# Optimization experiments

Measured on AMD Instinct MI355X. Metric: run time of the kernel, lower is better.

The kernel has to match this reference:

```python
import jax, jax.numpy as jnp
import numpy as np
import math

IN_C, OUT_C = 64, 128
OUT_C1 = int((OUT_C - IN_C) * 0.3 + IN_C)  # 83
OUT_C2 = int((OUT_C - IN_C) * 0.6 + IN_C)  # 102
OUT_C3 = OUT_C                              # 128
RESIDUE_RATIO = 0.5
R_RES = math.sqrt(RESIDUE_RATIO)
R_SC = math.sqrt(1.0 - RESIDUE_RATIO)
PRELU_INIT = 0.25
POST_MEAN = (1.0 - PRELU_INIT) / math.sqrt(2.0 * math.pi)
_POST_EX2 = (1.0 + PRELU_INIT ** 2) / 2.0
POST_STDV = math.sqrt(_POST_EX2 - POST_MEAN ** 2)


def _conv1x1_weight(key, out_c, in_c):
    # torch Conv1d custom init: normal_, then divide by per-out-channel L2 norm
    w = jax.random.normal(key, (out_c, in_c), dtype=jnp.float32)
    norm = jnp.sqrt(jnp.sum(w ** 2, axis=1, keepdims=True) + 1e-8)
    return w / norm


def cprelu(x, w):
    # x: [B, C, N], w: [C]
    y = jnp.where(x >= 0, x, x * w[None, :, None])
    return (y - POST_MEAN) / POST_STDV


def setup_inputs() -> dict:
    key = jax.random.key(0)
    ks = jax.random.split(key, 8)
    x = jax.random.normal(ks[0], (16, IN_C, 8192), dtype=jnp.float32)
    conn = jax.random.uniform(ks[1], (4096, 8192), dtype=jnp.float32)
    return {
        "x": x,
        "conn": conn,
        "w1": _conv1x1_weight(ks[2], OUT_C1, IN_C),
        "b1": jnp.zeros((OUT_C1,), jnp.float32),
        "p1": jnp.full((OUT_C1,), PRELU_INIT, jnp.float32),
        "w2": _conv1x1_weight(ks[3], OUT_C2, OUT_C1),
        "b2": jnp.zeros((OUT_C2,), jnp.float32),
        "p2": jnp.full((OUT_C2,), PRELU_INIT, jnp.float32),
        "wm": _conv1x1_weight(ks[4], OUT_C3, OUT_C2),
        "bm": jnp.zeros((OUT_C3,), jnp.float32),
        "p3": jnp.full((OUT_C3,), PRELU_INIT, jnp.float32),
        "ws": _conv1x1_weight(ks[5], OUT_C, IN_C),
        "bs": jnp.zeros((OUT_C,), jnp.float32),
    }


def _forward(x, conn, w1, b1, p1, w2, b2, p2, wm, bm, p3, ws, bs):
    # self-connection matrix: binary mask of per-row argmax entries (ties kept)
    sc = (conn - jnp.max(conn, axis=1, keepdims=True) >= 0).astype(jnp.float32)

    # residue branch: 1x1 conv -> CPReLU -> 1x1 conv -> CPReLU -> Meshconv -> CPReLU
    h = cprelu(jnp.einsum('bcn,oc->bon', x, w1) + b1[None, :, None], p1)
    h = cprelu(jnp.einsum('bcn,oc->bon', h, w2) + b2[None, :, None], p2)
    h = jnp.einsum('bcn,oc->bon', h, wm) + bm[None, :, None]      # [B, C3, Nin]
    h = jnp.einsum('oi,bci->bco', conn, h)                         # mesh pooling -> [B, C3, Nout]
    res = cprelu(h, p3)

    # shortcut branch: Meshconv with self_connection_matrix (1x1 conv + pooled gather)
    s = jnp.einsum('bcn,oc->bon', x, ws) + bs[None, :, None]       # [B, OUT_C, Nin]
    s = jnp.einsum('oi,bci->bco', sc, s)                           # [B, OUT_C, Nout]

    return s * R_SC + res * R_RES


def reference(x, conn, w1, b1, p1, w2, b2, p2, wm, bm, p3, ws, bs):
    return _forward(x, conn, w1, b1, p1, w2, b2, p2, wm, bm, p3, ws, bs)
```

## Files before the change

### kernel.cpp

```cpp
#include <hip/hip_runtime.h>
#include <hip/hip_bf16.h>
#include <stdint.h>

using bf16x8 = __attribute__((ext_vector_type(8))) __bf16;
using bf16x4 = __attribute__((ext_vector_type(4))) __bf16;
using f32x4  = __attribute__((ext_vector_type(4))) float;

typedef const uint32_t __attribute__((address_space(1)))* gas_ptr;
typedef uint32_t __attribute__((address_space(3)))* las_ptr;

__device__ __forceinline__ void load_lds16(const void* g, void* l) {
    __builtin_amdgcn_global_load_lds((gas_ptr)g, (las_ptr)l, 16, 0, 0);
}

#define PM  0.29920671030107454f
#define PIS 1.5046096f
#define RHALF 0.70710678118654752f

__global__ __launch_bounds__(256) void k_prep(const float* __restrict__ w1,
                                              const float* __restrict__ w2,
                                              const float* __restrict__ wm,
                                              const float* __restrict__ wsw,
                                              __bf16* __restrict__ W1p,
                                              __bf16* __restrict__ W2p,
                                              __bf16* __restrict__ WMp,
                                              __bf16* __restrict__ WSp)
{
    const int id = blockIdx.x * 256 + threadIdx.x;
    const int stride = gridDim.x * 256;
    for (int i = id; i < 96 * 64; i += stride) {
        int oc = i >> 6, ic = i & 63;
        W1p[i] = (__bf16)((oc < 83) ? w1[oc * 64 + ic] : 0.f);
    }
    for (int i = id; i < 112 * 96; i += stride) {
        int oc = i / 96, ic = i % 96;
        W2p[i] = (__bf16)((oc < 102 && ic < 83) ? w2[oc * 83 + ic] : 0.f);
    }
    for (int i = id; i < 128 * 128; i += stride) {
        int oc = i >> 7, ic = i & 127;
        WMp[i] = (__bf16)((ic < 102) ? wm[oc * 102 + ic] : 0.f);
    }
    for (int i = id; i < 128 * 64; i += stride) {
        WSp[i] = (__bf16)wsw[i];
    }
}

__global__ __launch_bounds__(256) void k_conv(const float* __restrict__ conn,
                                              __bf16* __restrict__ cb,
                                              size_t rowstride,
                                              int* __restrict__ cnt,
                                              int* __restrict__ idx)
{
    const int o = blockIdx.x;
    const int t = threadIdx.x;
    const float* row = conn + (size_t)o * 8192;
    float4 v[8];
    float m = -1e30f;
#pragma unroll
    for (int q = 0; q < 8; q++) {
        v[q] = *(const float4*)(row + (size_t)(q * 256 + t) * 4);
        m = fmaxf(m, fmaxf(fmaxf(v[q].x, v[q].y), fmaxf(v[q].z, v[q].w)));
    }
    __syncthreads();
    __bf16* drow = cb + (size_t)o * rowstride;
#pragma unroll
    for (int q = 0; q < 8; q++) {
        bf16x4 w;
        w[0] = (__bf16)v[q].x; w[1] = (__bf16)v[q].y;
        w[2] = (__bf16)v[q].z; w[3] = (__bf16)v[q].w;
        *(bf16x4*)(drow + (size_t)(q * 256 + t) * 4) = w;
    }
#pragma unroll
    for (int off = 32; off > 0; off >>= 1) m = fmaxf(m, __shfl_down(m, off, 64));
    __shared__ float wmax[4];
    __shared__ int scnt;
    if ((t & 63) == 0) wmax[t >> 6] = m;
    if (t == 0) scnt = 0;
    __syncthreads();
    const float rmax = fmaxf(fmaxf(wmax[0], wmax[1]), fmaxf(wmax[2], wmax[3]));
#pragma unroll
    for (int q = 0; q < 8; q++) {
        float vv[4] = {v[q].x, v[q].y, v[q].z, v[q].w};
#pragma unroll
        for (int e = 0; e < 4; e++) {
            if (vv[e] >= rmax) {
                int p = atomicAdd(&scnt, 1);
                if (p < 16) idx[o * 16 + p] = (q * 256 + t) * 4 + e;
            }
        }
    }
    __syncthreads();
    if (t == 0) cnt[o] = scnt < 16 ? scnt : 16;
}

template<int KS>
__device__ __forceinline__ f32x4 mfma_tile(const __bf16* __restrict__ W, int wstride, int mt,
                                           const __bf16* B, int bstride, int nt, int lane)
{
    f32x4 acc = {0.f, 0.f, 0.f, 0.f};
    const int l15 = lane & 15;
    const int kg  = (lane >> 4) << 3;
    const __bf16* wp = W + (mt * 16 + l15) * wstride + kg;
    const __bf16* bp = B + (nt * 16 + l15) * bstride + kg;
#pragma unroll
    for (int ks = 0; ks < KS; ks++) {
        bf16x8 av = *(const bf16x8*)(wp + ks * 32);
        bf16x8 bv = *(const bf16x8*)(bp + ks * 32);
        acc = __builtin_amdgcn_mfma_f32_16x16x32_bf16(av, bv, acc, 0, 0, 0);
    }
    return acc;
}

__global__ __launch_bounds__(256) void k_chain(
    const float* __restrict__ x,
    const float* __restrict__ b1, const float* __restrict__ p1,
    const float* __restrict__ b2, const float* __restrict__ p2,
    const float* __restrict__ bm, const float* __restrict__ bs,
    const __bf16* __restrict__ W1p, const __bf16* __restrict__ W2p,
    const __bf16* __restrict__ WMp, const __bf16* __restrict__ WSp,
    __bf16* __restrict__ h3, __bf16* __restrict__ s_t)
{
    __shared__ __bf16 buf0[64 * 136];
    __shared__ __bf16 un[128 * 72];
    __shared__ float  bl[672];
    __bf16* H1t  = un;
    __bf16* OutT = un;
    float* b1l = bl;       float* p1l = bl + 96;
    float* b2l = bl + 192; float* p2l = bl + 304;
    float* bml = bl + 416; float* bsl = bl + 544;

    const int t = threadIdx.x, lane = t & 63, wid = t >> 6;
    const int b = blockIdx.y;
    const int p0 = blockIdx.x * 64;

    for (int i = t; i < 96; i += 256)  { b1l[i] = (i < 83)  ? b1[i] : 0.f; p1l[i] = (i < 83)  ? p1[i] : 0.f; }
    for (int i = t; i < 112; i += 256) { b2l[i] = (i < 102) ? b2[i] : 0.f; p2l[i] = (i < 102) ? p2[i] : 0.f; }
    for (int i = t; i < 128; i += 256) { bml[i] = bm[i]; bsl[i] = bs[i]; }

    {
        const int p = t & 63;
        const int cg = t >> 6;
#pragma unroll 4
        for (int it = 0; it < 16; it++) {
            int c = it * 4 + cg;
            buf0[p * 72 + c] = (__bf16)x[((size_t)b * 64 + c) * 8192 + p0 + p];
        }
    }
    __syncthreads();

    const int quad4 = (lane >> 4) << 2;
    const int l15 = lane & 15;

    for (int tt = wid; tt < 32; tt += 4) {
        int mt = tt >> 2, nt = tt & 3;
        f32x4 a = mfma_tile<2>(WSp, 64, mt, buf0, 72, nt, lane);
        int ocb = mt * 16 + quad4;
        int pos = nt * 16 + l15;
        bf16x4 ov;
#pragma unroll
        for (int r = 0; r < 4; r++) ov[r] = (__bf16)(a[r] + bsl[ocb + r]);
        *(bf16x4*)(s_t + ((size_t)b * 8192 + p0 + pos) * 128 + ocb) = ov;
    }
    for (int tt = wid; tt < 24; tt += 4) {
        int mt = tt >> 2, nt = tt & 3;
        f32x4 a = mfma_tile<2>(W1p, 64, mt, buf0, 72, nt, lane);
        int ocb = mt * 16 + quad4;
        int pos = nt * 16 + l15;
        bf16x4 ov;
#pragma unroll
        for (int r = 0; r < 4; r++) {
            float v = a[r] + b1l[ocb + r];
            v = (v >= 0.f) ? v : v * p1l[ocb + r];
            ov[r] = (__bf16)((v - PM) * PIS);
        }
        *(bf16x4*)(&H1t[pos * 104 + ocb]) = ov;
    }
    __syncthreads();

    for (int tt = wid; tt < 28; tt += 4) {
        int mt = tt >> 2, nt = tt & 3;
        f32x4 a = mfma_tile<3>(W2p, 96, mt, H1t, 104, nt, lane);
        int ocb = mt * 16 + quad4;
        int pos = nt * 16 + l15;
        bf16x4 ov;
#pragma unroll
        for (int r = 0; r < 4; r++) {
            float v = a[r] + b2l[ocb + r];
            v = (v >= 0.f) ? v : v * p2l[ocb + r];
            ov[r] = (__bf16)((v - PM) * PIS);
        }
        *(bf16x4*)(&buf0[pos * 136 + ocb]) = ov;
    }
    for (int i = t; i < 64 * 16; i += 256) {
        int pos = i >> 4, c = 112 + (i & 15);
        buf0[pos * 136 + c] = (__bf16)0.f;
    }
    __syncthreads();

    for (int tt = wid; tt < 32; tt += 4) {
        int mt = tt >> 2, nt = tt & 3;
        f32x4 a = mfma_tile<4>(WMp, 128, mt, buf0, 136, nt, lane);
        int ocb = mt * 16 + quad4;
        int pos = nt * 16 + l15;
#pragma unroll
        for (int r = 0; r < 4; r++)
            OutT[(ocb + r) * 72 + pos] = (__bf16)(a[r] + bml[ocb + r]);
    }
    __syncthreads();

#pragma unroll
    for (int it = 0; it < 4; it++) {
        int lin = it * 256 + t;
        int ch = lin >> 3, pc = lin & 7;
        bf16x8 v = *(const bf16x8*)(OutT + ch * 72 + pc * 8);
        *(bf16x8*)(h3 + ((size_t)b * 128 + ch) * 8192 + p0 + pc * 8) = v;
    }
}

__global__ __launch_bounds__(256, 4) void k_gemm(const __bf16* __restrict__ A,
                                                 const __bf16* __restrict__ B,
                                                 size_t bstride,
                                                 float* __restrict__ C0,
                                                 float* __restrict__ C1,
                                                 int KH)
{
    __shared__ __bf16 la[128 * 64];
    __shared__ __bf16 lb[128 * 64];
    const int t = threadIdx.x;
    const int lane = t & 63;
    const int wid = t >> 6;
    const int tM = blockIdx.y * 128;
    const int tN = blockIdx.x * 128;
    const int kz = blockIdx.z;
    const int k0 = kz * KH;
    float* __restrict__ C = kz ? C1 : C0;
    const int wm2 = (wid & 1) * 64;
    const int wn2 = (wid >> 1) * 64;

    f32x4 acc[4][4];
    const f32x4 zero = {0.f, 0.f, 0.f, 0.f};
#pragma unroll
    for (int i = 0; i < 4; i++)
#pragma unroll
        for (int j = 0; j < 4; j++) acc[i][j] = zero;

    const int tr = t >> 3;
    const int sc = (t & 7) ^ (tr & 7);
    const __bf16* pA[4];
    const __bf16* pB[4];
#pragma unroll
    for (int i = 0; i < 4; i++) {
        pA[i] = A + (size_t)(tM + i * 32 + tr) * 8192 + k0 + sc * 8;
        pB[i] = B + (size_t)(tN + i * 32 + tr) * bstride + k0 + sc * 8;
    }

    const int l15 = lane & 15;
    const int q = lane >> 4;
    int aoff[4], boff[4];
#pragma unroll
    for (int i = 0; i < 4; i++) {
        int row = wm2 + i * 16 + l15;
        aoff[i] = row * 64 + ((q ^ (row & 7)) * 8);
    }
#pragma unroll
    for (int j = 0; j < 4; j++) {
        int row = wn2 + j * 16 + l15;
        boff[j] = row * 64 + ((q ^ (row & 7)) * 8);
    }

    const int iters = KH >> 6;
    for (int it = 0; it < iters; it++) {
#pragma unroll
        for (int i = 0; i < 4; i++) load_lds16(pA[i], la + (i * 256 + t) * 8);
#pragma unroll
        for (int i = 0; i < 4; i++) load_lds16(pB[i], lb + (i * 256 + t) * 8);
#pragma unroll
        for (int i = 0; i < 4; i++) { pA[i] += 64; pB[i] += 64; }
        __syncthreads();
#pragma unroll
        for (int ks = 0; ks < 2; ks++) {
            bf16x8 af[4], bfr[4];
#pragma unroll
            for (int i = 0; i < 4; i++) af[i]  = *(const bf16x8*)(la + (aoff[i] ^ (ks << 5)));
#pragma unroll
            for (int j = 0; j < 4; j++) bfr[j] = *(const bf16x8*)(lb + (boff[j] ^ (ks << 5)));
#pragma unroll
            for (int i = 0; i < 4; i++)
#pragma unroll
                for (int j = 0; j < 4; j++)
                    acc[i][j] = __builtin_amdgcn_mfma_f32_16x16x32_bf16(af[i], bfr[j], acc[i][j], 0, 0, 0);
        }
        __syncthreads();
    }

    const int quad4 = (lane >> 4) * 4;
#pragma unroll
    for (int i = 0; i < 4; i++) {
        int gm = tM + wm2 + i * 16 + quad4;
#pragma unroll
        for (int j = 0; j < 4; j++) {
            int gn = tN + wn2 + j * 16 + l15;
#pragma unroll
            for (int r = 0; r < 4; r++)
                C[(size_t)(gm + r) * 4096 + gn] = acc[i][j][r];
        }
    }
}

__global__ __launch_bounds__(256) void k_combine(float* __restrict__ out,
                                                 const float* __restrict__ P1,
                                                 int nsplit,
                                                 const __bf16* __restrict__ s_t,
                                                 const int* __restrict__ idx,
                                                 const int* __restrict__ cnt,
                                                 const float* __restrict__ p3)
{
    __shared__ float sp[64][133];
    const int b = blockIdx.y;
    const int o0 = blockIdx.x * 64;
    const int t = threadIdx.x;

    {
        const int ol = t >> 2;
        const int part = t & 3;
        const int o = o0 + ol;
        const int n = cnt[o];
        float acc[32];
#pragma unroll
        for (int j = 0; j < 32; j++) acc[j] = 0.f;
        for (int k = 0; k < n; k++) {
            const int i = idx[o * 16 + k];
            const __bf16* row = s_t + ((size_t)b * 8192 + i) * 128 + part * 32;
#pragma unroll
            for (int j = 0; j < 32; j += 8) {
                bf16x8 v = *(const bf16x8*)(row + j);
#pragma unroll
                for (int u = 0; u < 8; u++) acc[j + u] += (float)v[u];
            }
        }
#pragma unroll
        for (int j = 0; j < 32; j++) sp[ol][part * 32 + j] = acc[j];
    }
    __syncthreads();

    if (nsplit == 2) {
        for (int rr = 0; rr < 32; rr++) {
            const int c = rr * 4 + (t >> 6);
            const int o = t & 63;
            const size_t oi = ((size_t)b * 128 + c) * 4096 + o0 + o;
            float v = out[oi] + P1[oi];
            const float pw = p3[c];
            float y = (v >= 0.f) ? v : v * pw;
            y = (y - PM) * PIS;
            out[oi] = sp[o][c] * RHALF + y * RHALF;
        }
    } else {
        for (int rr = 0; rr < 32; rr++) {
            const int c = rr * 4 + (t >> 6);
            const int o = t & 63;
            const size_t oi = ((size_t)b * 128 + c) * 4096 + o0 + o;
            float v = out[oi];
            const float pw = p3[c];
            float y = (v >= 0.f) ? v : v * pw;
            y = (y - PM) * PIS;
            out[oi] = sp[o][c] * RHALF + y * RHALF;
        }
    }
}

extern "C" void kernel_launch(void* const* d_in, const int* in_sizes, int n_in,
                              void* d_out, int out_size, void* d_ws, size_t ws_size,
                              hipStream_t stream) {
    (void)in_sizes; (void)n_in; (void)out_size;
    const float* x    = (const float*)d_in[0];
    const float* conn = (const float*)d_in[1];
    const float* w1   = (const float*)d_in[2];
    const float* b1   = (const float*)d_in[3];
    const float* p1   = (const float*)d_in[4];
    const float* w2   = (const float*)d_in[5];
    const float* b2   = (const float*)d_in[6];
    const float* p2   = (const float*)d_in[7];
    const float* wm   = (const float*)d_in[8];
    const float* bm   = (const float*)d_in[9];
    const float* p3   = (const float*)d_in[10];
    const float* wsw  = (const float*)d_in[11];
    const float* bs   = (const float*)d_in[12];
    float* out = (float*)d_out;

    char* ws = (char*)d_ws;
    __bf16* h3  = (__bf16*)(ws);
    __bf16* s_t = (__bf16*)(ws + 33554432);
    __bf16* W1p = (__bf16*)(ws + 67108864);
    __bf16* W2p = (__bf16*)(ws + 67108864 + 12288);
    __bf16* WMp = (__bf16*)(ws + 67108864 + 33792);
    __bf16* WSp = (__bf16*)(ws + 67108864 + 66560);
    int* idx = (int*)(ws + 67108864 + 82944);
    int* cnt = (int*)(ws + 67108864 + 82944 + 262144);
    const size_t p1_off    = 67108864 + 82944 + 262144 + 16384;
    float* Pk1 = (float*)(ws + p1_off);
    const size_t connb_off = p1_off + 33554432;

    __bf16* connb;
    size_t  cstride;
    if (ws_size >= connb_off + (size_t)4096 * 8192 * 2) {
        connb = (__bf16*)(ws + connb_off);
        cstride = 8192;
    } else {
        connb = (__bf16*)const_cast<float*>(conn);
        cstride = 16384;
    }
    const int nsplit = (ws_size >= p1_off + 33554432) ? 2 : 1;
    const int KH = 8192 / nsplit;

    k_prep<<<32, 256, 0, stream>>>(w1, w2, wm, wsw, W1p, W2p, WMp, WSp);
    k_conv<<<4096, 256, 0, stream>>>(conn, connb, cstride, cnt, idx);
    k_chain<<<dim3(8192 / 64, 16), 256, 0, stream>>>(x, b1, p1, b2, p2, bm, bs,
                                                     W1p, W2p, WMp, WSp, h3, s_t);
    k_gemm<<<dim3(4096 / 128, 2048 / 128, nsplit), 256, 0, stream>>>(h3, connb, cstride,
                                                                     out, Pk1, KH);
    k_combine<<<dim3(4096 / 64, 16), 256, 0, stream>>>(out, Pk1, nsplit, s_t, idx, cnt, p3);
}
```

Baseline: 485.8 us.

## Split GEMM K four ways, fuse weight prep, stage shortcut stores, vectorize combine

Several changes land together. The weight-prep kernel is folded into the conn conversion kernel, which removes one launch. The shortcut output is staged through LDS so global writes become contiguous 16-byte stores. The main GEMM's K split goes from 2 to 4 when the workspace allows, which adds more blocks but also more partial buffers that must be read back. The combine epilogue is vectorized to float4 and sums up to four partials.

```diff
diff --git a/kernel.cpp b/kernel.cpp
--- a/kernel.cpp
+++ b/kernel.cpp
@@ -17,7 +17,12 @@
 #define PIS 1.5046096f
 #define RHALF 0.70710678118654752f
 
-__global__ __launch_bounds__(256) void k_prep(const float* __restrict__ w1,
+__global__ __launch_bounds__(256) void k_conv(const float* __restrict__ conn,
+                                              __bf16* __restrict__ cb,
+                                              size_t rowstride,
+                                              int* __restrict__ cnt,
+                                              int* __restrict__ idx,
+                                              const float* __restrict__ w1,
                                               const float* __restrict__ w2,
                                               const float* __restrict__ wm,
                                               const float* __restrict__ wsw,
@@ -26,31 +31,6 @@
                                               __bf16* __restrict__ WMp,
                                               __bf16* __restrict__ WSp)
 {
-    const int id = blockIdx.x * 256 + threadIdx.x;
-    const int stride = gridDim.x * 256;
-    for (int i = id; i < 96 * 64; i += stride) {
-        int oc = i >> 6, ic = i & 63;
-        W1p[i] = (__bf16)((oc < 83) ? w1[oc * 64 + ic] : 0.f);
-    }
-    for (int i = id; i < 112 * 96; i += stride) {
-        int oc = i / 96, ic = i % 96;
-        W2p[i] = (__bf16)((oc < 102 && ic < 83) ? w2[oc * 83 + ic] : 0.f);
-    }
-    for (int i = id; i < 128 * 128; i += stride) {
-        int oc = i >> 7, ic = i & 127;
-        WMp[i] = (__bf16)((ic < 102) ? wm[oc * 102 + ic] : 0.f);
-    }
-    for (int i = id; i < 128 * 64; i += stride) {
-        WSp[i] = (__bf16)wsw[i];
-    }
-}
-
-__global__ __launch_bounds__(256) void k_conv(const float* __restrict__ conn,
-                                              __bf16* __restrict__ cb,
-                                              size_t rowstride,
-                                              int* __restrict__ cnt,
-                                              int* __restrict__ idx)
-{
     const int o = blockIdx.x;
     const int t = threadIdx.x;
     const float* row = conn + (size_t)o * 8192;
@@ -91,6 +71,26 @@
     }
     __syncthreads();
     if (t == 0) cnt[o] = scnt < 16 ? scnt : 16;
+
+    if (o < 32) {
+        const int id = o * 256 + t;
+        const int stride = 32 * 256;
+        for (int i = id; i < 96 * 64; i += stride) {
+            int oc = i >> 6, ic = i & 63;
+            W1p[i] = (__bf16)((oc < 83) ? w1[oc * 64 + ic] : 0.f);
+        }
+        for (int i = id; i < 112 * 96; i += stride) {
+            int oc = i / 96, ic = i % 96;
+            W2p[i] = (__bf16)((oc < 102 && ic < 83) ? w2[oc * 83 + ic] : 0.f);
+        }
+        for (int i = id; i < 128 * 128; i += stride) {
+            int oc = i >> 7, ic = i & 127;
+            WMp[i] = (__bf16)((ic < 102) ? wm[oc * 102 + ic] : 0.f);
+        }
+        for (int i = id; i < 128 * 64; i += stride) {
+            WSp[i] = (__bf16)wsw[i];
+        }
+    }
 }
 
 template<int KS>
@@ -123,6 +123,7 @@
     __shared__ __bf16 buf0[64 * 136];
     __shared__ __bf16 un[128 * 72];
     __shared__ float  bl[672];
+    __bf16* OutS = un;
     __bf16* H1t  = un;
     __bf16* OutT = un;
     float* b1l = bl;       float* p1l = bl + 96;
@@ -159,8 +160,21 @@
         bf16x4 ov;
 #pragma unroll
         for (int r = 0; r < 4; r++) ov[r] = (__bf16)(a[r] + bsl[ocb + r]);
-        *(bf16x4*)(s_t + ((size_t)b * 8192 + p0 + pos) * 128 + ocb) = ov;
-    }
+        *(bf16x4*)(&OutS[pos * 132 + ocb]) = ov;
+    }
+    __syncthreads();
+    {
+        __bf16* dst = s_t + ((size_t)b * 8192 + p0) * 128;
+#pragma unroll
+        for (int it = 0; it < 4; it++) {
+            int lin = it * 256 + t;
+            int pos = lin >> 4, c8 = (lin & 15) * 8;
+            bf16x8 v = *(const bf16x8*)(OutS + pos * 132 + c8);
+            *(bf16x8*)(dst + lin * 8) = v;
+        }
+    }
+    __syncthreads();
+
     for (int tt = wid; tt < 24; tt += 4) {
         int mt = tt >> 2, nt = tt & 3;
         f32x4 a = mfma_tile<2>(W1p, 64, mt, buf0, 72, nt, lane);
@@ -221,7 +235,9 @@
                                                  const __bf16* __restrict__ B,
                                                  size_t bstride,
                                                  float* __restrict__ C0,
-                                                 float* __restrict__ C1,
+                                                 float* __restrict__ P1,
+                                                 float* __restrict__ P2,
+                                                 float* __restrict__ P3,
                                                  int KH)
 {
     __shared__ __bf16 la[128 * 64];
@@ -233,7 +249,8 @@
     const int tN = blockIdx.x * 128;
     const int kz = blockIdx.z;
     const int k0 = kz * KH;
-    float* __restrict__ C = kz ? C1 : C0;
+    float* __restrict__ C = C0;
+    if (kz == 1) C = P1; else if (kz == 2) C = P2; else if (kz == 3) C = P3;
     const int wm2 = (wid & 1) * 64;
     const int wn2 = (wid >> 1) * 64;
 
@@ -309,7 +326,9 @@
 
 __global__ __launch_bounds__(256) void k_combine(float* __restrict__ out,
                                                  const float* __restrict__ P1,
-                                                 int nsplit,
+                                                 const float* __restrict__ P2,
+                                                 const float* __restrict__ P3,
+                                                 int ns,
                                                  const __bf16* __restrict__ s_t,
                                                  const int* __restrict__ idx,
                                                  const int* __restrict__ cnt,
@@ -343,28 +362,35 @@
     }
     __syncthreads();
 
-    if (nsplit == 2) {
-        for (int rr = 0; rr < 32; rr++) {
-            const int c = rr * 4 + (t >> 6);
-            const int o = t & 63;
-            const size_t oi = ((size_t)b * 128 + c) * 4096 + o0 + o;
-            float v = out[oi] + P1[oi];
-            const float pw = p3[c];
-            float y = (v >= 0.f) ? v : v * pw;
+    const int ol4 = (t & 15) * 4;
+    const int cbase = t >> 4;
+#pragma unroll
+    for (int cc = 0; cc < 8; cc++) {
+        const int c = cc * 16 + cbase;
+        const size_t oi = ((size_t)b * 128 + c) * 4096 + o0 + ol4;
+        float4 v = *(const float4*)(out + oi);
+        if (ns >= 2) {
+            float4 a = *(const float4*)(P1 + oi);
+            v.x += a.x; v.y += a.y; v.z += a.z; v.w += a.w;
+        }
+        if (ns >= 4) {
+            float4 a2 = *(const float4*)(P2 + oi);
+            float4 a3 = *(const float4*)(P3 + oi);
+            v.x += a2.x + a3.x; v.y += a2.y + a3.y;
+            v.z += a2.z + a3.z; v.w += a2.w + a3.w;
+        }
+        const float pw = p3[c];
+        float4 r;
+        float vv[4] = {v.x, v.y, v.z, v.w};
+        float rr[4];
+#pragma unroll
+        for (int e = 0; e < 4; e++) {
+            float y = (vv[e] >= 0.f) ? vv[e] : vv[e] * pw;
             y = (y - PM) * PIS;
-            out[oi] = sp[o][c] * RHALF + y * RHALF;
-        }
-    } else {
-        for (int rr = 0; rr < 32; rr++) {
-            const int c = rr * 4 + (t >> 6);
-            const int o = t & 63;
-            const size_t oi = ((size_t)b * 128 + c) * 4096 + o0 + o;
-            float v = out[oi];
-            const float pw = p3[c];
-            float y = (v >= 0.f) ? v : v * pw;
-            y = (y - PM) * PIS;
-            out[oi] = sp[o][c] * RHALF + y * RHALF;
-        }
+            rr[e] = sp[ol4 + e][c] * RHALF + y * RHALF;
+        }
+        r.x = rr[0]; r.y = rr[1]; r.z = rr[2]; r.w = rr[3];
+        *(float4*)(out + oi) = r;
     }
 }
 
@@ -396,27 +422,38 @@
     __bf16* WSp = (__bf16*)(ws + 67108864 + 66560);
     int* idx = (int*)(ws + 67108864 + 82944);
     int* cnt = (int*)(ws + 67108864 + 82944 + 262144);
-    const size_t p1_off    = 67108864 + 82944 + 262144 + 16384;
-    float* Pk1 = (float*)(ws + p1_off);
-    const size_t connb_off = p1_off + 33554432;
+    const size_t pbase = 67108864 + 82944 + 262144 + 16384;
+    const size_t psz = 33554432;
+    const size_t connb_sz = (size_t)4096 * 8192 * 2;
+
+    int nsplit; bool conn_ws;
+    if      (ws_size >= pbase + 3 * psz + connb_sz) { nsplit = 4; conn_ws = true;  }
+    else if (ws_size >= pbase + 3 * psz)            { nsplit = 4; conn_ws = false; }
+    else if (ws_size >= pbase + 1 * psz + connb_sz) { nsplit = 2; conn_ws = true;  }
+    else if (ws_size >= pbase + 1 * psz)            { nsplit = 2; conn_ws = false; }
+    else { nsplit = 1; conn_ws = (ws_size >= pbase + connb_sz); }
+
+    float* Pk1 = (float*)(ws + pbase);
+    float* Pk2 = (float*)(ws + pbase + psz);
+    float* Pk3 = (float*)(ws + pbase + 2 * psz);
 
     __bf16* connb;
     size_t  cstride;
-    if (ws_size >= connb_off + (size_t)4096 * 8192 * 2) {
-        connb = (__bf16*)(ws + connb_off);
+    if (conn_ws) {
+        connb = (__bf16*)(ws + pbase + (size_t)(nsplit - 1) * psz);
         cstride = 8192;
     } else {
         connb = (__bf16*)const_cast<float*>(conn);
         cstride = 16384;
     }
-    const int nsplit = (ws_size >= p1_off + 33554432) ? 2 : 1;
     const int KH = 8192 / nsplit;
 
-    k_prep<<<32, 256, 0, stream>>>(w1, w2, wm, wsw, W1p, W2p, WMp, WSp);
-    k_conv<<<4096, 256, 0, stream>>>(conn, connb, cstride, cnt, idx);
+    k_conv<<<4096, 256, 0, stream>>>(conn, connb, cstride, cnt, idx,
+                                     w1, w2, wm, wsw, W1p, W2p, WMp, WSp);
     k_chain<<<dim3(8192 / 64, 16), 256, 0, stream>>>(x, b1, p1, b2, p2, bm, bs,
                                                      W1p, W2p, WMp, WSp, h3, s_t);
     k_gemm<<<dim3(4096 / 128, 2048 / 128, nsplit), 256, 0, stream>>>(h3, connb, cstride,
-                                                                     out, Pk1, KH);
-    k_combine<<<dim3(4096 / 64, 16), 256, 0, stream>>>(out, Pk1, nsplit, s_t, idx, cnt, p3);
-}
+                                                                     out, Pk1, Pk2, Pk3, KH);
+    k_combine<<<dim3(4096 / 64, 16), 256, 0, stream>>>(out, Pk1, Pk2, Pk3, nsplit,
+                                                       s_t, idx, cnt, p3);
+}
```

After: 493.6 us. No clear change (+1.6%).
